# Optimization experiments

Measured on AMD Instinct MI355X. Metric: run time of the kernel, lower is better.

## Reference

```python
import jax, jax.numpy as jnp
import numpy as np

# Dimensions (match init_kwargs / input_specs)
B, C, H, W = 16, 16, 64, 64
N = H * W          # num_nodes
D_E = 64           # node_embed_dim
D_H = 128          # gnn_hidden_dim
D_R = 256          # readout_output_dim


def _param(key, shape, fan_in):
    return jax.random.normal(key, shape, jnp.float32) * (1.0 / np.sqrt(fan_in))


def setup_inputs() -> dict:
    key = jax.random.key(0)
    ks = jax.random.split(key, 16)
    inp = {
        "obs": jax.random.normal(ks[0], (B, C, H, W), jnp.float32),
        # node_embedding MLP (2 layers: C -> D_E -> D_E)
        "e1_w": _param(ks[1], (C, D_E), C),   "e1_b": jnp.zeros((D_E,), jnp.float32),
        "e2_w": _param(ks[2], (D_E, D_E), D_E), "e2_b": jnp.zeros((D_E,), jnp.float32),
        # 3 GNN layers (Linear then adjacency aggregation)
        "g1_w": _param(ks[3], (D_E, D_H), D_E), "g1_b": jnp.zeros((D_H,), jnp.float32),
        "g2_w": _param(ks[4], (D_H, D_H), D_H), "g2_b": jnp.zeros((D_H,), jnp.float32),
        "g3_w": _param(ks[5], (D_H, D_H), D_H), "g3_b": jnp.zeros((D_H,), jnp.float32),
        # readout MLP (2 layers: D_H -> 2*D_H -> D_R)
        "r1_w": _param(ks[6], (D_H, 2 * D_H), D_H),   "r1_b": jnp.zeros((2 * D_H,), jnp.float32),
        "r2_w": _param(ks[7], (2 * D_H, D_R), 2 * D_H), "r2_b": jnp.zeros((D_R,), jnp.float32),
    }
    return inp


def _adj_norm():
    # 4-neighbor grid adjacency on an H x W grid, row-normalized (same for every
    # batch element, so build once as (N, N) instead of (B, N, N)).
    idx = jnp.arange(N)
    up = jnp.eye(N, k=-W, dtype=jnp.float32)                      # i > 0
    down = jnp.eye(N, k=W, dtype=jnp.float32)                     # i < H-1
    left = jnp.eye(N, k=-1, dtype=jnp.float32) * ((idx % W) != 0)[:, None]
    right = jnp.eye(N, k=1, dtype=jnp.float32) * ((idx % W) != (W - 1))[:, None]
    adj = up + down + left + right
    return adj / (adj.sum(axis=1, keepdims=True) + 1e-6)


def reference(obs, e1_w, e1_b, e2_w, e2_b,
              g1_w, g1_b, g2_w, g2_b, g3_w, g3_b,
              r1_w, r1_b, r2_w, r2_b):
    relu = jax.nn.relu
    # grid -> graph: (B, C, H, W) -> (B, N, C)
    x = jnp.transpose(obs, (0, 2, 3, 1)).reshape(B, N, C)
    # node embedding MLP (output activation per ding MLP default)
    h = relu(x @ e1_w + e1_b)
    h = relu(h @ e2_w + e2_b)
    A = _adj_norm()  # (N, N)
    for Wg, bg in ((g1_w, g1_b), (g2_w, g2_b), (g3_w, g3_b)):
        support = h @ Wg + bg                      # (B, N, D_H)
        h = relu(jnp.einsum('nm,bmf->bnf', A, support))
    g = h.mean(axis=1)                              # (B, D_H) graph readout
    g = relu(g @ r1_w + r1_b)
    return relu(g @ r2_w + r2_b)                    # (B, D_R)
```

## Files before the change

kernel.cpp:

```cpp
#include <hip/hip_runtime.h>


typedef __attribute__((ext_vector_type(8))) short bf16x8;
typedef __attribute__((ext_vector_type(4))) float f32x4;
#define MFMA(a, b, c) __builtin_amdgcn_mfma_f32_16x16x32_bf16(a, b, c, 0, 0, 0)

__device__ inline void block_sync_lgkm() {
    asm volatile("" ::: "memory");
    __builtin_amdgcn_s_waitcnt(0xC07F);
    __builtin_amdgcn_s_barrier();
    asm volatile("" ::: "memory");
}

__device__ inline ushort bf16h(float x) {
    unsigned u = __float_as_uint(x);
    return (ushort)((u + 0x7fffu + ((u >> 16) & 1u)) >> 16);
}
__device__ inline void split_bf16(float x, ushort& hi, ushort& lo) {
    hi = bf16h(x);
    lo = bf16h(x - __uint_as_float(((unsigned)hi) << 16));
}
__device__ inline unsigned pack_split(float x) {
    unsigned u = __float_as_uint(x);
    unsigned hi = (u + 0x7fffu + ((u >> 16) & 1u)) >> 16;
    float r = x - __uint_as_float(hi << 16);
    return (hi << 16) | (__float_as_uint(r) >> 16);
}
__device__ inline void frag_packed(const unsigned* bp, bf16x8& bh, bf16x8& bl) {
    unsigned p[8];
#pragma unroll
    for (int j = 0; j < 8; j++) p[j] = bp[j * 65];
    union { bf16x8 v; unsigned d[4]; } H, L;
#pragma unroll
    for (int j = 0; j < 4; j++) {
        const unsigned e = p[2 * j], o = p[2 * j + 1];
        H.d[j] = (o & 0xFFFF0000u) | (e >> 16);
        L.d[j] = (o << 16) | (e & 0xFFFFu);
    }
    bh = H.v; bl = L.v;
}

__global__ __launch_bounds__(256, 4) void prep_embed_kernel(
    const float* __restrict__ obs,
    const float* __restrict__ e1w, const float* __restrict__ e1b,
    const float* __restrict__ e2w, const float* __restrict__ e2b,
    const float* __restrict__ g1w, const float* __restrict__ g2w,
    const float* __restrict__ g3w, ushort* __restrict__ wf,
    float* __restrict__ gsum, float* __restrict__ h0)
{
    const int blk = blockIdx.x, tid = threadIdx.x;

    if (blk < 20) {
        const int u = blk * 4 + (tid >> 6);
        const int l = tid & 63;
        const float* src; int K, kc, t; ushort* dst;
        if (u < 16)      { src = g1w; K = 64;  kc = u >> 3;        t = u & 7; dst = wf + 12288; }
        else if (u < 48) { src = g2w; K = 128; kc = (u - 16) >> 3; t = (u - 16) & 7; dst = wf + 28672; }
        else             { src = g3w; K = 128; kc = (u - 48) >> 3; t = (u - 48) & 7; dst = wf + 61440; }
        ushort* uh = dst + ((kc * 8 + t) * 2 + 0) * 512 + l * 8;
        ushort* ul = dst + ((kc * 8 + t) * 2 + 1) * 512 + l * 8;
        const int f = t * 16 + (l & 15);
        const int kb = kc * 32 + ((l >> 4) << 3);
#pragma unroll
        for (int j = 0; j < 8; j++) {
            const int k = kb + j;
            const float w = (k < K) ? src[k * 128 + f] : 0.f;
            ushort hi, lo; split_bf16(w, hi, lo);
            uh[j] = hi; ul[j] = lo;
        }
        return;
    }
    if (blk < 28) {
        gsum[(blk - 20) * 256 + tid] = 0.f;
        return;
    }

    __shared__ unsigned lds[6240];
    const int eb = blk - 28, b = eb >> 6, row = eb & 63;
    const int lane = tid & 63, w = tid >> 6, quad = lane >> 4, nl = lane & 15;
    const int cp = tid >> 4, nq = tid & 15;

    const float4 x4 = *(const float4*)(obs + ((size_t)(b * 16 + cp) << 12) + row * 64 + nq * 4);

    {
        float* wr = (float*)lds;
#pragma unroll
        for (int i = 0; i < 20; i++) {
            const int idx = tid + 256 * i;
            wr[idx] = (idx < 1024) ? e1w[idx] : e2w[idx - 1024];
        }
    }
    __syncthreads();

    bf16x8 e1h, e1l, e2h[2], e2l[2];
    {
        const float* wr = (const float*)lds;
        const int f = 16 * w + nl;
#pragma unroll
        for (int j = 0; j < 8; j++) {
            const int k = quad * 8 + j;
            const float v = (k < 16) ? wr[k * 64 + f] : 0.f;
            ushort hi, lo; split_bf16(v, hi, lo);
            e1h[j] = (short)hi; e1l[j] = (short)lo;
        }
#pragma unroll
        for (int kc = 0; kc < 2; kc++)
#pragma unroll
            for (int j = 0; j < 8; j++) {
                const int k = kc * 32 + quad * 8 + j;
                const float v = wr[1024 + k * 64 + f];
                ushort hi, lo; split_bf16(v, hi, lo);
                e2h[kc][j] = (short)hi; e2l[kc][j] = (short)lo;
            }
    }
    __syncthreads();

    unsigned* Xs = lds;
    unsigned* Hs = lds + 2080;
    {
        unsigned* xp = Xs + cp * 65 + nq * 4;
        xp[0] = pack_split(x4.x); xp[1] = pack_split(x4.y);
        xp[2] = pack_split(x4.z); xp[3] = pack_split(x4.w);
        unsigned* zp = Xs + (16 + cp) * 65 + nq * 4;
        zp[0] = 0u; zp[1] = 0u; zp[2] = 0u; zp[3] = 0u;
    }
    __syncthreads();

#pragma unroll
    for (int nt = 0; nt < 4; nt++) {
        const unsigned* bp = Xs + (quad * 8) * 65 + nt * 16 + nl;
        bf16x8 bh, bl; frag_packed(bp, bh, bl);
        f32x4 c = {0.f, 0.f, 0.f, 0.f};
        c = MFMA(e1h, bh, c); c = MFMA(e1h, bl, c); c = MFMA(e1l, bh, c);
#pragma unroll
        for (int reg = 0; reg < 4; reg++) {
            const int fm = 16 * w + quad * 4 + reg;
            Hs[fm * 65 + nt * 16 + nl] = pack_split(fmaxf(c[reg] + e1b[fm], 0.f));
        }
    }
    __syncthreads();

    f32x4 a2[4];
#pragma unroll
    for (int nt = 0; nt < 4; nt++) a2[nt] = (f32x4){0.f, 0.f, 0.f, 0.f};
#pragma unroll
    for (int kc = 0; kc < 2; kc++) {
#pragma unroll
        for (int nt = 0; nt < 4; nt++) {
            const unsigned* bp = Hs + (kc * 32 + quad * 8) * 65 + nt * 16 + nl;
            bf16x8 bh, bl; frag_packed(bp, bh, bl);
            a2[nt] = MFMA(e2h[kc], bh, a2[nt]);
            a2[nt] = MFMA(e2h[kc], bl, a2[nt]);
            a2[nt] = MFMA(e2l[kc], bh, a2[nt]);
        }
    }
#pragma unroll
    for (int reg = 0; reg < 4; reg++) {
        const int f = 16 * w + quad * 4 + reg;
        const float bv = e2b[f];
#pragma unroll
        for (int nt = 0; nt < 4; nt++)
            h0[((size_t)(b * 64 + f) << 12) + row * 64 + nt * 16 + nl] =
                fmaxf(a2[nt][reg] + bv, 0.f);
    }
}

template <int K, bool MEAN>
__global__ __launch_bounds__(256, 4) void gnn_kernel(
    const float* __restrict__ hin, const ushort* __restrict__ wf,
    const float* __restrict__ bias, float* __restrict__ hout,
    float* __restrict__ gsum)
{
    constexpr int NQ = K / 32;
    __shared__ unsigned As[2][32 * 65];
    const int tid = threadIdx.x;
    const int bid = ((blockIdx.x & 7) << 7) | (blockIdx.x >> 3);
    const int b = bid >> 6, row = bid & 63;
    const int lane = tid & 63, w = tid >> 6, quad = lane >> 4, nl = lane & 15;
    const int kp = tid >> 4, nq = tid & 15;
    const float* hb = hin + (size_t)b * K * 4096;
    const int rowu = (row > 0) ? row - 1 : row;
    const int rowd = (row < 63) ? row + 1 : row;
    const float su = (row > 0) ? 1.f : 0.f;
    const float sd = (row < 63) ? 1.f : 0.f;
    float inv[4];
#pragma unroll
    for (int i = 0; i < 4; i++) {
        const int n = nq * 4 + i;
        const int deg = (row > 0) + (row < 63) + (n > 0) + (n < 63);
        inv[i] = 1.f / ((float)deg + 1e-6f);
    }

    const ushort* wfl = wf + lane * 8;
    f32x4 acc[4][2];
#pragma unroll
    for (int nt = 0; nt < 4; nt++) {
        acc[nt][0] = (f32x4){0.f, 0.f, 0.f, 0.f};
        acc[nt][1] = (f32x4){0.f, 0.f, 0.f, 0.f};
    }

    float4 S[6];
    bf16x8 V[2][2];

    auto sload = [&](int q) {
#pragma unroll
        for (int it = 0; it < 2; it++) {
            const int kg = q * 32 + it * 16 + kp;
            const float* pk = hb + ((size_t)kg << 12) + nq * 4;
            S[it * 3 + 0] = *(const float4*)(pk + row * 64);
            S[it * 3 + 1] = *(const float4*)(pk + rowu * 64);
            S[it * 3 + 2] = *(const float4*)(pk + rowd * 64);
        }
    };
    auto wload = [&](int q) {
#pragma unroll
        for (int ftl = 0; ftl < 2; ftl++) {
            V[ftl][0] = *(const bf16x8*)(wfl + ((q * 8 + 2 * w + ftl) * 2) * 512);
            V[ftl][1] = *(const bf16x8*)(wfl + ((q * 8 + 2 * w + ftl) * 2 + 1) * 512);
        }
    };
    auto stage = [&](unsigned* Ab) {
#pragma unroll
        for (int it = 0; it < 2; it++) {
            const int kl = it * 16 + kp;
            const float4 c4 = S[it * 3 + 0];
            const float4 u4 = S[it * 3 + 1];
            const float4 d4 = S[it * 3 + 2];
            const float pw = __shfl_up(c4.w, 1);
            const float nx = __shfl_down(c4.x, 1);
            const float lx = (nq > 0) ? pw : 0.f;
            const float rw = (nq < 15) ? nx : 0.f;
            unsigned* ap = Ab + kl * 65 + nq * 4;
            ap[0] = pack_split((su * u4.x + sd * d4.x + lx + c4.y) * inv[0]);
            ap[1] = pack_split((su * u4.y + sd * d4.y + c4.x + c4.z) * inv[1]);
            ap[2] = pack_split((su * u4.z + sd * d4.z + c4.y + c4.w) * inv[2]);
            ap[3] = pack_split((su * u4.w + sd * d4.w + c4.z + rw) * inv[3]);
        }
    };
    auto consume = [&](const unsigned* Ab) {
#pragma unroll
        for (int nt = 0; nt < 4; nt++) {
            const unsigned* bp = Ab + (quad * 8) * 65 + nt * 16 + nl;
            bf16x8 bh, bl; frag_packed(bp, bh, bl);
            acc[nt][0] = MFMA(V[0][0], bh, acc[nt][0]);
            acc[nt][0] = MFMA(V[0][0], bl, acc[nt][0]);
            acc[nt][0] = MFMA(V[0][1], bh, acc[nt][0]);
            acc[nt][1] = MFMA(V[1][0], bh, acc[nt][1]);
            acc[nt][1] = MFMA(V[1][0], bl, acc[nt][1]);
            acc[nt][1] = MFMA(V[1][1], bh, acc[nt][1]);
        }
    };

    wload(0);
    sload(0);
    stage(As[0]);
    sload(1);
    block_sync_lgkm();

#pragma unroll
    for (int q = 0; q < NQ; q++) {
        consume(As[q & 1]);
        if (q + 1 < NQ) {
            wload(q + 1);
            stage(As[(q + 1) & 1]);
            if (q + 2 < NQ) sload(q + 2);
            block_sync_lgkm();
        }
    }

    if (!MEAN) {
#pragma unroll
        for (int ftl = 0; ftl < 2; ftl++) {
            const int fb = 32 * w + 16 * ftl + quad * 4;
            const float b0 = bias[fb], b1 = bias[fb + 1], b2 = bias[fb + 2], b3 = bias[fb + 3];
#pragma unroll
            for (int nt = 0; nt < 4; nt++) {
                const int n = 16 * nt + nl;
                const int deg = (row > 0) + (row < 63) + (n > 0) + (n < 63);
                const float rs = (float)deg / ((float)deg + 1e-6f);
                float* op = hout + ((size_t)(b * 128 + fb) << 12) + row * 64 + n;
                op[0]        = fmaxf(acc[nt][ftl][0] + rs * b0, 0.f);
                op[1u << 12] = fmaxf(acc[nt][ftl][1] + rs * b1, 0.f);
                op[2u << 12] = fmaxf(acc[nt][ftl][2] + rs * b2, 0.f);
                op[3u << 12] = fmaxf(acc[nt][ftl][3] + rs * b3, 0.f);
            }
        }
    } else {
#pragma unroll
        for (int ftl = 0; ftl < 2; ftl++) {
            const int fb = 32 * w + 16 * ftl + quad * 4;
#pragma unroll
            for (int reg = 0; reg < 4; reg++) {
                const float bv = bias[fb + reg];
                float v = 0.f;
#pragma unroll
                for (int nt = 0; nt < 4; nt++) {
                    const int n = 16 * nt + nl;
                    const int deg = (row > 0) + (row < 63) + (n > 0) + (n < 63);
                    const float rs = (float)deg / ((float)deg + 1e-6f);
                    v += fmaxf(acc[nt][ftl][reg] + rs * bv, 0.f);
                }
                v += __shfl_xor(v, 1); v += __shfl_xor(v, 2);
                v += __shfl_xor(v, 4); v += __shfl_xor(v, 8);
                if (nl == 0) atomicAdd(&gsum[b * 128 + fb + reg], v * (1.f / 4096.f));
            }
        }
    }
}

__global__ __launch_bounds__(256) void readout_kernel(
    const float* __restrict__ gsum, const float* __restrict__ r1w,
    const float* __restrict__ r1b, const float* __restrict__ r2w,
    const float* __restrict__ r2b, float* __restrict__ out)
{
    __shared__ float gs[128];
    __shared__ float g2[256];
    const int b = blockIdx.x, tid = threadIdx.x;
    if (tid < 128) gs[tid] = gsum[b * 128 + tid];
    __syncthreads();
    float a = r1b[tid];
#pragma unroll 16
    for (int k = 0; k < 128; k++) a = fmaf(gs[k], r1w[k * 256 + tid], a);
    g2[tid] = fmaxf(a, 0.f);
    __syncthreads();
    float a2 = r2b[tid];
#pragma unroll 16
    for (int k = 0; k < 256; k++) a2 = fmaf(g2[k], r2w[k * 256 + tid], a2);
    out[b * 256 + tid] = fmaxf(a2, 0.f);
}

extern "C" void kernel_launch(void* const* d_in, const int* in_sizes, int n_in,
                              void* d_out, int out_size, void* d_ws, size_t ws_size,
                              hipStream_t stream)
{
    const float* obs = (const float*)d_in[0];
    const float* e1w = (const float*)d_in[1];
    const float* e1b = (const float*)d_in[2];
    const float* e2w = (const float*)d_in[3];
    const float* e2b = (const float*)d_in[4];
    const float* g1w = (const float*)d_in[5];
    const float* g1b = (const float*)d_in[6];
    const float* g2w = (const float*)d_in[7];
    const float* g2b = (const float*)d_in[8];
    const float* g3w = (const float*)d_in[9];
    const float* g3b = (const float*)d_in[10];
    const float* r1w = (const float*)d_in[11];
    const float* r1b = (const float*)d_in[12];
    const float* r2w = (const float*)d_in[13];
    const float* r2b = (const float*)d_in[14];
    float* out = (float*)d_out;
    float* ws = (float*)d_ws;

    float* h0 = ws;
    float* h1 = ws + 4194304;
    float* h2 = ws + 4194304 + 8388608;
    float* gsum = (float*)((char*)d_ws + 80u * 1024u * 1024u);
    ushort* wfb = (ushort*)((char*)d_ws + 80u * 1024u * 1024u + 8192u);

    hipLaunchKernelGGL(prep_embed_kernel, dim3(1052), dim3(256), 0, stream,
                       obs, e1w, e1b, e2w, e2b, g1w, g2w, g3w, wfb, gsum, h0);
    hipLaunchKernelGGL((gnn_kernel<64, false>), dim3(1024), dim3(256), 0, stream,
                       h0, wfb + 12288, g1b, h1, nullptr);
    hipLaunchKernelGGL((gnn_kernel<128, false>), dim3(1024), dim3(256), 0, stream,
                       h1, wfb + 28672, g2b, h2, nullptr);
    hipLaunchKernelGGL((gnn_kernel<128, true>), dim3(1024), dim3(256), 0, stream,
                       h2, wfb + 61440, g3b, nullptr, gsum);
    hipLaunchKernelGGL(readout_kernel, dim3(16), dim3(256), 0, stream,
                       gsum, r1w, r1b, r2w, r2b, out);
}
```

Measured before the change: 160.4 us.

## Fuse node embedding MLP into first GNN layer with halo row recompute

```diff
diff --git a/kernel.cpp b/kernel.cpp
--- a/kernel.cpp
+++ b/kernel.cpp
@@ -4,13 +4,6 @@
 typedef __attribute__((ext_vector_type(8))) short bf16x8;
 typedef __attribute__((ext_vector_type(4))) float f32x4;
 #define MFMA(a, b, c) __builtin_amdgcn_mfma_f32_16x16x32_bf16(a, b, c, 0, 0, 0)
-
-__device__ inline void block_sync_lgkm() {
-    asm volatile("" ::: "memory");
-    __builtin_amdgcn_s_waitcnt(0xC07F);
-    __builtin_amdgcn_s_barrier();
-    asm volatile("" ::: "memory");
-}
 
 __device__ inline ushort bf16h(float x) {
     unsigned u = __float_as_uint(x);
@@ -40,50 +33,57 @@
     bh = H.v; bl = L.v;
 }
 
-__global__ __launch_bounds__(256, 4) void prep_embed_kernel(
+__global__ __launch_bounds__(256) void wprep_kernel(
+    const float* __restrict__ g1w, const float* __restrict__ g2w,
+    const float* __restrict__ g3w, ushort* __restrict__ wf,
+    float* __restrict__ gsum)
+{
+    const int blk = blockIdx.x, tid = threadIdx.x;
+    if (blk >= 20) {
+        gsum[(blk - 20) * 256 + tid] = 0.f;
+        return;
+    }
+    const int u = blk * 4 + (tid >> 6);
+    const int l = tid & 63;
+    const float* src; int K, kc, t; ushort* dst;
+    if (u < 16)      { src = g1w; K = 64;  kc = u >> 3;        t = u & 7; dst = wf + 12288; }
+    else if (u < 48) { src = g2w; K = 128; kc = (u - 16) >> 3; t = (u - 16) & 7; dst = wf + 28672; }
+    else             { src = g3w; K = 128; kc = (u - 48) >> 3; t = (u - 48) & 7; dst = wf + 61440; }
+    ushort* uh = dst + ((kc * 8 + t) * 2 + 0) * 512 + l * 8;
+    ushort* ul = dst + ((kc * 8 + t) * 2 + 1) * 512 + l * 8;
+    const int f = t * 16 + (l & 15);
+    const int kb = kc * 32 + ((l >> 4) << 3);
+#pragma unroll
+    for (int j = 0; j < 8; j++) {
+        const int k = kb + j;
+        const float w = (k < K) ? src[k * 128 + f] : 0.f;
+        ushort hi, lo; split_bf16(w, hi, lo);
+        uh[j] = hi; ul[j] = lo;
+    }
+}
+
+__global__ __launch_bounds__(256, 2) void fused_eg1_kernel(
     const float* __restrict__ obs,
     const float* __restrict__ e1w, const float* __restrict__ e1b,
     const float* __restrict__ e2w, const float* __restrict__ e2b,
-    const float* __restrict__ g1w, const float* __restrict__ g2w,
-    const float* __restrict__ g3w, ushort* __restrict__ wf,
-    float* __restrict__ gsum, float* __restrict__ h0)
+    const ushort* __restrict__ g1f, const float* __restrict__ g1b,
+    float* __restrict__ h1)
 {
-    const int blk = blockIdx.x, tid = threadIdx.x;
-
-    if (blk < 20) {
-        const int u = blk * 4 + (tid >> 6);
-        const int l = tid & 63;
-        const float* src; int K, kc, t; ushort* dst;
-        if (u < 16)      { src = g1w; K = 64;  kc = u >> 3;        t = u & 7; dst = wf + 12288; }
-        else if (u < 48) { src = g2w; K = 128; kc = (u - 16) >> 3; t = (u - 16) & 7; dst = wf + 28672; }
-        else             { src = g3w; K = 128; kc = (u - 48) >> 3; t = (u - 48) & 7; dst = wf + 61440; }
-        ushort* uh = dst + ((kc * 8 + t) * 2 + 0) * 512 + l * 8;
-        ushort* ul = dst + ((kc * 8 + t) * 2 + 1) * 512 + l * 8;
-        const int f = t * 16 + (l & 15);
-        const int kb = kc * 32 + ((l >> 4) << 3);
-#pragma unroll
-        for (int j = 0; j < 8; j++) {
-            const int k = kb + j;
-            const float w = (k < K) ? src[k * 128 + f] : 0.f;
-            ushort hi, lo; split_bf16(w, hi, lo);
-            uh[j] = hi; ul[j] = lo;
-        }
-        return;
-    }
-    if (blk < 28) {
-        gsum[(blk - 20) * 256 + tid] = 0.f;
-        return;
-    }
-
-    __shared__ unsigned lds[6240];
-    const int eb = blk - 28, b = eb >> 6, row = eb & 63;
+    __shared__ __align__(16) unsigned lds[12544 + 6240];
+    float* h0s = (float*)lds;
+    unsigned* scr = lds + 12544;
+    const int tid = threadIdx.x;
+    const int bid = ((blockIdx.x & 7) << 7) | (blockIdx.x >> 3);
+    const int b = bid >> 6, row = bid & 63;
     const int lane = tid & 63, w = tid >> 6, quad = lane >> 4, nl = lane & 15;
     const int cp = tid >> 4, nq = tid & 15;
-
-    const float4 x4 = *(const float4*)(obs + ((size_t)(b * 16 + cp) << 12) + row * 64 + nq * 4);
+    const int rowu = (row > 0) ? row - 1 : row;
+    const int rowd = (row < 63) ? row + 1 : row;
+    const float su = (row > 0) ? 1.f : 0.f;
+    const float sd = (row < 63) ? 1.f : 0.f;
 
     {
-        float* wr = (float*)lds;
+        float* wr = (float*)scr;
 #pragma unroll
         for (int i = 0; i < 20; i++) {
             const int idx = tid + 256 * i;
@@ -91,10 +91,9 @@
         }
     }
     __syncthreads();
-
     bf16x8 e1h, e1l, e2h[2], e2l[2];
     {
-        const float* wr = (const float*)lds;
+        const float* wr = (const float*)scr;
         const int f = 16 * w + nl;
 #pragma unroll
         for (int j = 0; j < 8; j++) {
@@ -115,54 +114,130 @@
     }
     __syncthreads();
 
-    unsigned* Xs = lds;
-    unsigned* Hs = lds + 2080;
-    {
+    unsigned* Xs = scr;
+    unsigned* Hs = scr + 2080;
+    const int rsel[3] = { rowu, row, rowd };
+#pragma unroll 1
+    for (int ri = 0; ri < 3; ri++) {
+        const int r = rsel[ri];
+        const float4 x4 = *(const float4*)(obs + ((size_t)(b * 16 + cp) << 12) + r * 64 + nq * 4);
         unsigned* xp = Xs + cp * 65 + nq * 4;
         xp[0] = pack_split(x4.x); xp[1] = pack_split(x4.y);
         xp[2] = pack_split(x4.z); xp[3] = pack_split(x4.w);
         unsigned* zp = Xs + (16 + cp) * 65 + nq * 4;
         zp[0] = 0u; zp[1] = 0u; zp[2] = 0u; zp[3] = 0u;
+        __syncthreads();
+
+#pragma unroll
+        for (int nt = 0; nt < 4; nt++) {
+            const unsigned* bp = Xs + (quad * 8) * 65 + nt * 16 + nl;
+            bf16x8 bh, bl; frag_packed(bp, bh, bl);
+            f32x4 c = {0.f, 0.f, 0.f, 0.f};
+            c = MFMA(e1h, bh, c); c = MFMA(e1h, bl, c); c = MFMA(e1l, bh, c);
+#pragma unroll
+            for (int reg = 0; reg < 4; reg++) {
+                const int fm = 16 * w + quad * 4 + reg;
+                Hs[fm * 65 + nt * 16 + nl] = pack_split(fmaxf(c[reg] + e1b[fm], 0.f));
+            }
+        }
+        __syncthreads();
+
+        f32x4 a2[4];
+#pragma unroll
+        for (int nt = 0; nt < 4; nt++) a2[nt] = (f32x4){0.f, 0.f, 0.f, 0.f};
+#pragma unroll
+        for (int kc = 0; kc < 2; kc++) {
+#pragma unroll
+            for (int nt = 0; nt < 4; nt++) {
+                const unsigned* bp = Hs + (kc * 32 + quad * 8) * 65 + nt * 16 + nl;
+                bf16x8 bh, bl; frag_packed(bp, bh, bl);
+                a2[nt] = MFMA(e2h[kc], bh, a2[nt]);
+                a2[nt] = MFMA(e2h[kc], bl, a2[nt]);
+                a2[nt] = MFMA(e2l[kc], bh, a2[nt]);
+            }
+        }
+#pragma unroll
+        for (int reg = 0; reg < 4; reg++) {
+            const int f = 16 * w + quad * 4 + reg;
+            const float bv = e2b[f];
+#pragma unroll
+            for (int nt = 0; nt < 4; nt++)
+                h0s[f * 196 + ri * 64 + nt * 16 + nl] = fmaxf(a2[nt][reg] + bv, 0.f);
+        }
+        __syncthreads();
+    }
+
+    const ushort* wfl = g1f + lane * 8;
+    bf16x8 V[2][2][2];
+#pragma unroll
+    for (int kc = 0; kc < 2; kc++)
+#pragma unroll
+        for (int ftl = 0; ftl < 2; ftl++) {
+            V[kc][ftl][0] = *(const bf16x8*)(wfl + ((kc * 8 + 2 * w + ftl) * 2) * 512);
+            V[kc][ftl][1] = *(const bf16x8*)(wfl + ((kc * 8 + 2 * w + ftl) * 2 + 1) * 512);
+        }
+
+    unsigned* As = scr;
+    {
+        const int n = lane;
+        const int deg = (row > 0) + (row < 63) + (n > 0) + (n < 63);
+        const float inv1 = 1.f / ((float)deg + 1e-6f);
+        const float sl = (n > 0) ? 1.f : 0.f;
+        const float sr = (n < 63) ? 1.f : 0.f;
+#pragma unroll
+        for (int it = 0; it < 16; it++) {
+            const int k = w + it * 4;
+            const float* hr = h0s + k * 196;
+            const float s = su * hr[n] + sd * hr[128 + n]
+                          + sl * hr[63 + n] + sr * hr[65 + n];
+            As[k * 65 + n] = pack_split(s * inv1);
+        }
     }
     __syncthreads();
 
+    f32x4 acc[4][2];
 #pragma unroll
     for (int nt = 0; nt < 4; nt++) {
-        const unsigned* bp = Xs + (quad * 8) * 65 + nt * 16 + nl;
-        bf16x8 bh, bl; frag_packed(bp, bh, bl);
-        f32x4 c = {0.f, 0.f, 0.f, 0.f};
-        c = MFMA(e1h, bh, c); c = MFMA(e1h, bl, c); c = MFMA(e1l, bh, c);
-#pragma unroll
-        for (int reg = 0; reg < 4; reg++) {
-            const int fm = 16 * w + quad * 4 + reg;
-            Hs[fm * 65 + nt * 16 + nl] = pack_split(fmaxf(c[reg] + e1b[fm], 0.f));
-        }
-    }
-    __syncthreads();
-
-    f32x4 a2[4];
-#pragma unroll
-    for (int nt = 0; nt < 4; nt++) a2[nt] = (f32x4){0.f, 0.f, 0.f, 0.f};
+        acc[nt][0] = (f32x4){0.f, 0.f, 0.f, 0.f};
+        acc[nt][1] = (f32x4){0.f, 0.f, 0.f, 0.f};
+    }
 #pragma unroll
     for (int kc = 0; kc < 2; kc++) {
 #pragma unroll
         for (int nt = 0; nt < 4; nt++) {
-            const unsigned* bp = Hs + (kc * 32 + quad * 8) * 65 + nt * 16 + nl;
+            const unsigned* bp = As + (kc * 32 + quad * 8) * 65 + nt * 16 + nl;
             bf16x8 bh, bl; frag_packed(bp, bh, bl);
-            a2[nt] = MFMA(e2h[kc], bh, a2[nt]);
-            a2[nt] = MFMA(e2h[kc], bl, a2[nt]);
-            a2[nt] = MFMA(e2l[kc], bh, a2[nt]);
-        }
-    }
-#pragma unroll
-    for (int reg = 0; reg < 4; reg++) {
-        const int f = 16 * w + quad * 4 + reg;
-        const float bv = e2b[f];
-#pragma unroll
-        for (int nt = 0; nt < 4; nt++)
-            h0[((size_t)(b * 64 + f) << 12) + row * 64 + nt * 16 + nl] =
-                fmaxf(a2[nt][reg] + bv, 0.f);
-    }
+            acc[nt][0] = MFMA(V[kc][0][0], bh, acc[nt][0]);
+            acc[nt][0] = MFMA(V[kc][0][0], bl, acc[nt][0]);
+            acc[nt][0] = MFMA(V[kc][0][1], bh, acc[nt][0]);
+            acc[nt][1] = MFMA(V[kc][1][0], bh, acc[nt][1]);
+            acc[nt][1] = MFMA(V[kc][1][0], bl, acc[nt][1]);
+            acc[nt][1] = MFMA(V[kc][1][1], bh, acc[nt][1]);
+        }
+    }
+#pragma unroll
+    for (int ftl = 0; ftl < 2; ftl++) {
+        const int fb = 32 * w + 16 * ftl + quad * 4;
+        const float b0 = g1b[fb], b1 = g1b[fb + 1], b2 = g1b[fb + 2], b3 = g1b[fb + 3];
+#pragma unroll
+        for (int nt = 0; nt < 4; nt++) {
+            const int n = 16 * nt + nl;
+            const int deg = (row > 0) + (row < 63) + (n > 0) + (n < 63);
+            const float rs = (float)deg / ((float)deg + 1e-6f);
+            float* op = h1 + ((size_t)(b * 128 + fb) << 12) + row * 64 + n;
+            op[0]        = fmaxf(acc[nt][ftl][0] + rs * b0, 0.f);
+            op[1u << 12] = fmaxf(acc[nt][ftl][1] + rs * b1, 0.f);
+            op[2u << 12] = fmaxf(acc[nt][ftl][2] + rs * b2, 0.f);
+            op[3u << 12] = fmaxf(acc[nt][ftl][3] + rs * b3, 0.f);
+        }
+    }
+}
+
+__device__ inline void block_sync_lgkm() {
+    asm volatile("" ::: "memory");
+    __builtin_amdgcn_s_waitcnt(0xC07F);
+    __builtin_amdgcn_s_barrier();
+    asm volatile("" ::: "memory");
 }
 
 template <int K, bool MEAN>
@@ -351,16 +426,15 @@
     float* out = (float*)d_out;
     float* ws = (float*)d_ws;
 
-    float* h0 = ws;
     float* h1 = ws + 4194304;
     float* h2 = ws + 4194304 + 8388608;
     float* gsum = (float*)((char*)d_ws + 80u * 1024u * 1024u);
     ushort* wfb = (ushort*)((char*)d_ws + 80u * 1024u * 1024u + 8192u);
 
-    hipLaunchKernelGGL(prep_embed_kernel, dim3(1052), dim3(256), 0, stream,
-                       obs, e1w, e1b, e2w, e2b, g1w, g2w, g3w, wfb, gsum, h0);
-    hipLaunchKernelGGL((gnn_kernel<64, false>), dim3(1024), dim3(256), 0, stream,
-                       h0, wfb + 12288, g1b, h1, nullptr);
+    hipLaunchKernelGGL(wprep_kernel, dim3(28), dim3(256), 0, stream,
+                       g1w, g2w, g3w, wfb, gsum);
+    hipLaunchKernelGGL(fused_eg1_kernel, dim3(1024), dim3(256), 0, stream,
+                       obs, e1w, e1b, e2w, e2b, wfb + 12288, g1b, h1);
     hipLaunchKernelGGL((gnn_kernel<128, false>), dim3(1024), dim3(256), 0, stream,
                        h1, wfb + 28672, g2b, h2, nullptr);
     hipLaunchKernelGGL((gnn_kernel<128, true>), dim3(1024), dim3(256), 0, stream,
```

Result: slower. 171.7 us (+7.0%).
